# Kernel tuning notes

Hardware: AMD Instinct MI355X
Metric: run time of the kernel (lower is better)

The kernel has to match this reference:

```python
import jax, jax.numpy as jnp
import numpy as np
from math import sqrt

B, LQ, LKV = 4, 1024, 1024
QD = KD = VD = 1024
MODEL_DIM = 1024
H = 16
HD = MODEL_DIM // H  # per-head model_dim = 64


def setup_inputs() -> dict:
    key = jax.random.key(0)
    ks = jax.random.split(key, 10)
    s = 0.02
    return {
        "queries": jax.random.normal(ks[0], (B, LQ, QD), jnp.float32),
        "context": jax.random.normal(ks[1], (B, LKV, KD), jnp.float32),
        # stacked per-head linear weights (torch Linear: y = x @ W.T + b); store as [H, in, out]
        "Wq": jax.random.normal(ks[2], (H, QD, HD), jnp.float32) * s,
        "bq": jax.random.normal(ks[3], (H, HD), jnp.float32) * s,
        "Wk": jax.random.normal(ks[4], (KD, HD * 1 * H), jnp.float32).reshape(H, KD, HD) * s,
        "bk": jax.random.normal(ks[5], (H, HD), jnp.float32) * s,
        "Wv": jax.random.normal(ks[6], (H, VD, HD), jnp.float32) * s,
        "bv": jax.random.normal(ks[7], (H, HD), jnp.float32) * s,
        "Wo": jax.random.normal(ks[8], (H * HD, MODEL_DIM), jnp.float32) * s,
        "bo": jax.random.normal(ks[9], (MODEL_DIM,), jnp.float32) * s,
    }


def reference(queries, context, Wq, bq, Wk, bk, Wv, bv, Wo, bo):
    # queries: [B,Lq,Dq]; context: [B,Lkv,Dk]
    # Per-head projections, batched over heads (equivalent to the torch per-head loop).
    q = jnp.einsum("bld,hdm->bhlm", queries, Wq) + bq[None, :, None, :]  # [B,H,Lq,hd]
    k = jnp.einsum("bld,hdm->bhlm", context, Wk) + bk[None, :, None, :]  # [B,H,Lkv,hd]
    v = jnp.einsum("bld,hdm->bhlm", context, Wv) + bv[None, :, None, :]  # [B,H,Lkv,hd]

    scale = 1.0 / sqrt(HD)
    scores = jnp.einsum("bhqd,bhkd->bhqk", q, k) * scale  # [B,H,Lq,Lkv]
    att = jax.nn.softmax(scores, axis=-1)
    head_out = jnp.einsum("bhqk,bhkd->bhqd", att, v)  # [B,H,Lq,hd]

    # torch concatenates heads along the last dim in head order 0..H-1
    multi = head_out.transpose(0, 2, 1, 3).reshape(B, LQ, H * HD)
    residual = q.transpose(0, 2, 1, 3).reshape(B, LQ, H * HD)

    out = multi @ Wo + bo  # [B,Lq,model_dim]
    return out, residual
```

## Files before the change

kernel.cpp:

```cpp
#include <hip/hip_runtime.h>
#include <hip/hip_bf16.h>


typedef unsigned short u16;
typedef __attribute__((ext_vector_type(8))) short short8;
typedef __attribute__((ext_vector_type(4))) float f32x4;

__device__ __forceinline__ float bf2f(u16 u) {
    union { unsigned int i; float f; } c;
    c.i = ((unsigned int)u) << 16;
    return c.f;
}

__device__ __forceinline__ u16 f2bf(float f) {
    unsigned int x = __float_as_uint(f);
    unsigned int r = (x + 0x7fffu + ((x >> 16) & 1u)) >> 16;
    return (u16)r;
}

__device__ __forceinline__ void glds16(u16* lds, const u16* g) {
    __builtin_amdgcn_global_load_lds(
        (const __attribute__((address_space(1))) void*)g,
        (__attribute__((address_space(3))) void*)lds, 16, 0, 0);
}

__global__ __launch_bounds__(256) void cast_bf16_kernel(
    const float* __restrict__ q, const float* __restrict__ c,
    u16* __restrict__ oq, u16* __restrict__ oc)
{
    const float* in = blockIdx.y ? c : q;
    u16* out = blockIdx.y ? oc : oq;
    size_t i = ((size_t)blockIdx.x * 256 + threadIdx.x) * 8;
    float4 v0 = *(const float4*)(in + i);
    float4 v1 = *(const float4*)(in + i + 4);
    short8 p;
    p[0] = (short)f2bf(v0.x); p[1] = (short)f2bf(v0.y);
    p[2] = (short)f2bf(v0.z); p[3] = (short)f2bf(v0.w);
    p[4] = (short)f2bf(v1.x); p[5] = (short)f2bf(v1.y);
    p[6] = (short)f2bf(v1.z); p[7] = (short)f2bf(v1.w);
    *(short8*)(out + i) = p;
}

__global__ __launch_bounds__(256) void transpose_cast(
    const float* __restrict__ in, u16* __restrict__ out, int C, size_t matStride)
{
    __shared__ float ls[64][65];
    const int t = threadIdx.x;
    const size_t moff = (size_t)blockIdx.z * matStride;
    const int rt = blockIdx.x * 64, ct = blockIdx.y * 64;
    #pragma unroll
    for (int i = 0; i < 4; ++i) {
        int s = i * 256 + t;
        int row = s >> 4, chunk = s & 15;
        float4 v = *(const float4*)(in + moff + (size_t)(rt + row) * C + ct + chunk * 4);
        ls[row][chunk * 4 + 0] = v.x;
        ls[row][chunk * 4 + 1] = v.y;
        ls[row][chunk * 4 + 2] = v.z;
        ls[row][chunk * 4 + 3] = v.w;
    }
    __syncthreads();
    #pragma unroll
    for (int i = 0; i < 2; ++i) {
        int s = i * 256 + t;
        int n = s >> 3, kc = s & 7;
        short8 p;
        #pragma unroll
        for (int j = 0; j < 8; ++j) p[j] = (short)f2bf(ls[kc * 8 + j][n]);
        *(short8*)(out + moff + (size_t)(ct + n) * 1024 + rt + kc * 8) = p;
    }
}

__device__ __forceinline__ void gemm_core(
    const u16* __restrict__ A, const u16* __restrict__ Wt,
    int m0, u16* As, u16* Bs, f32x4 (&acc)[4][4])
{
    const int t = threadIdx.x;
    const int w = t >> 6, lane = t & 63;
    const int quad = lane >> 4, c = lane & 15;
    const int srow = w * 32 + (lane >> 2);
    const int sch = lane & 3;

    const u16* gA = A + (size_t)(m0 + srow) * 1024 + sch * 8;
    const u16* gB = Wt + (size_t)srow * 1024 + sch * 8;
    u16* lA = As + w * 32 * 32;
    u16* lB = Bs + w * 32 * 32;
    const u16* afr = As + ((w >> 1) * 64 + c) * 32 + quad * 8;
    const u16* bfr = Bs + ((w & 1) * 64 + c) * 32 + quad * 8;

    for (int kt = 0; kt < 1024; kt += 32) {
        glds16(lA,           gA + kt);
        glds16(lA + 16 * 32, gA + kt + 16 * 1024);
        glds16(lB,           gB + kt);
        glds16(lB + 16 * 32, gB + kt + 16 * 1024);
        __syncthreads();
        short8 af[4], bf[4];
        #pragma unroll
        for (int rs = 0; rs < 4; ++rs) af[rs] = *(const short8*)(afr + rs * 16 * 32);
        #pragma unroll
        for (int cs = 0; cs < 4; ++cs) bf[cs] = *(const short8*)(bfr + cs * 16 * 32);
        #pragma unroll
        for (int rs = 0; rs < 4; ++rs)
            #pragma unroll
            for (int cs = 0; cs < 4; ++cs)
                acc[rs][cs] = __builtin_amdgcn_mfma_f32_16x16x32_bf16(
                    af[rs], bf[cs], acc[rs][cs], 0, 0, 0);
        __syncthreads();
    }
}

__global__ __launch_bounds__(256, 3) void gemm_qkv(
    const u16* __restrict__ Aq, const u16* __restrict__ Ac,
    const u16* __restrict__ Wqt, const u16* __restrict__ Wkt,
    const u16* __restrict__ Wvt,
    const float* __restrict__ bq, const float* __restrict__ bk,
    const float* __restrict__ bv,
    u16* __restrict__ qws, u16* __restrict__ kws, u16* __restrict__ vtws,
    float* __restrict__ resid)
{
    __shared__ u16 As[128 * 32];
    __shared__ u16 Bs[128 * 32];
    const int n0 = blockIdx.x * 128, m0 = blockIdx.y * 128, z = blockIdx.z;
    const int t = threadIdx.x;
    const int w = t >> 6, lane = t & 63;
    const int quad = lane >> 4, c = lane & 15;

    const u16* A = (z == 0) ? Aq : Ac;
    const u16* Wt = ((z == 0) ? Wqt : (z == 1) ? Wkt : Wvt) + (size_t)n0 * 1024;
    const float* bias = (z == 0) ? bq : (z == 1) ? bk : bv;

    f32x4 acc[4][4] = {};
    gemm_core(A, Wt, m0, As, Bs, acc);

    const int h = blockIdx.x * 2 + (w & 1);
    float bb[4];
    #pragma unroll
    for (int cs = 0; cs < 4; ++cs) bb[cs] = bias[h * 64 + cs * 16 + c];

    if (z == 2) {
        #pragma unroll
        for (int rs = 0; rs < 4; ++rs) {
            const int l0 = m0 + (w >> 1) * 64 + rs * 16 + quad * 4;
            const int b = l0 >> 10, l = l0 & 1023;
            #pragma unroll
            for (int cs = 0; cs < 4; ++cs) {
                const int hd = cs * 16 + c;
                ushort4 pk;
                pk.x = f2bf(acc[rs][cs][0] + bb[cs]);
                pk.y = f2bf(acc[rs][cs][1] + bb[cs]);
                pk.z = f2bf(acc[rs][cs][2] + bb[cs]);
                pk.w = f2bf(acc[rs][cs][3] + bb[cs]);
                *(ushort4*)(vtws + ((size_t)(b * 16 + h) * 64 + hd) * 1024 + l) = pk;
            }
        }
    } else {
        u16* dst = (z == 0) ? qws : kws;
        const float scale = (z == 0) ? 0.125f : 1.0f;
        #pragma unroll
        for (int rs = 0; rs < 4; ++rs) {
            #pragma unroll
            for (int r = 0; r < 4; ++r) {
                const int row = m0 + (w >> 1) * 64 + rs * 16 + quad * 4 + r;
                const int b = row >> 10, l = row & 1023;
                u16* drow = dst + (((size_t)(b * 16 + h) * 1024) + l) * 64;
                float* rrow = (z == 0) ? (resid + (size_t)row * 1024 + h * 64) : nullptr;
                #pragma unroll
                for (int cs = 0; cs < 4; ++cs) {
                    float v = acc[rs][cs][r] + bb[cs];
                    drow[cs * 16 + c] = f2bf(v * scale);
                    if (z == 0) rrow[cs * 16 + c] = v;
                }
            }
        }
    }
}

__global__ __launch_bounds__(256, 3) void gemm_out(
    const u16* __restrict__ A, const u16* __restrict__ Wot,
    const float* __restrict__ bo, float* __restrict__ out)
{
    __shared__ u16 As[128 * 32];
    __shared__ u16 Bs[128 * 32];
    const int n0 = blockIdx.x * 128, m0 = blockIdx.y * 128;
    const int t = threadIdx.x;
    const int w = t >> 6, lane = t & 63;
    const int quad = lane >> 4, c = lane & 15;

    f32x4 acc[4][4] = {};
    gemm_core(A, Wot + (size_t)n0 * 1024, m0, As, Bs, acc);

    const int nb = n0 + (w & 1) * 64;
    float bb[4];
    #pragma unroll
    for (int cs = 0; cs < 4; ++cs) bb[cs] = bo[nb + cs * 16 + c];

    #pragma unroll
    for (int rs = 0; rs < 4; ++rs) {
        #pragma unroll
        for (int r = 0; r < 4; ++r) {
            const int row = m0 + (w >> 1) * 64 + rs * 16 + quad * 4 + r;
            float* orow = out + (size_t)row * 1024 + nb;
            #pragma unroll
            for (int cs = 0; cs < 4; ++cs)
                orow[cs * 16 + c] = acc[rs][cs][r] + bb[cs];
        }
    }
}

__global__ __launch_bounds__(256, 4) void attn_mfma(
    const u16* __restrict__ qws, const u16* __restrict__ kws,
    const u16* __restrict__ vtws, u16* __restrict__ multi)
{
    __shared__ u16 Ks[64 * 64];
    __shared__ u16 Vs[64 * 64];
    __shared__ u16 Ps[4][16 * 72];
    const int t = threadIdx.x;
    const int wave = t >> 6, lane = t & 63;
    const int quad = lane >> 4, c = lane & 15;
    const int bh = blockIdx.y, b = bh >> 4, h = bh & 15;
    const int q0 = blockIdx.x * 64 + wave * 16;

    const u16* qb = qws + ((size_t)bh * 1024 + q0) * 64;
    const u16* kb = kws + (size_t)bh * 65536;
    const u16* vb = vtws + (size_t)bh * 65536;

    short8 qa0 = *(const short8*)(qb + (size_t)c * 64 + quad * 8);
    short8 qa1 = *(const short8*)(qb + (size_t)c * 64 + 32 + quad * 8);

    const int srow = wave * 16 + (lane >> 3);
    const int gch = (lane & 7) ^ ((lane >> 3) & 7);
    u16* ldsK0 = Ks + (wave * 16) * 64;
    u16* ldsK1 = Ks + (wave * 16 + 8) * 64;
    u16* ldsV0 = Vs + (wave * 16) * 64;
    u16* ldsV1 = Vs + (wave * 16 + 8) * 64;
    const u16* gK0 = kb + (size_t)srow * 64 + gch * 8;
    const u16* gK1 = kb + (size_t)(srow + 8) * 64 + gch * 8;
    const u16* gV0 = vb + (size_t)srow * 1024 + gch * 8;
    const u16* gV1 = vb + (size_t)(srow + 8) * 1024 + gch * 8;

    f32x4 O[4] = {};
    float ps[4] = {0.f, 0.f, 0.f, 0.f};
    u16* pw = &Ps[wave][0];
    const int cx = c & 7;

    for (int kt = 0; kt < 1024; kt += 64) {
        glds16(ldsK0, gK0 + (size_t)kt * 64);
        glds16(ldsK1, gK1 + (size_t)kt * 64);
        glds16(ldsV0, gV0 + kt);
        glds16(ldsV1, gV1 + kt);
        __syncthreads();

        f32x4 s[4];
        #pragma unroll
        for (int nt = 0; nt < 4; ++nt) {
            const u16* kr = Ks + (nt * 16 + c) * 64;
            short8 kb0 = *(const short8*)(kr + ((quad ^ cx)) * 8);
            short8 kb1 = *(const short8*)(kr + (((4 + quad) ^ cx)) * 8);
            f32x4 z = {};
            z = __builtin_amdgcn_mfma_f32_16x16x32_bf16(qa0, kb0, z, 0, 0, 0);
            z = __builtin_amdgcn_mfma_f32_16x16x32_bf16(qa1, kb1, z, 0, 0, 0);
            s[nt] = z;
        }

        #pragma unroll
        for (int nt = 0; nt < 4; ++nt)
            #pragma unroll
            for (int r = 0; r < 4; ++r) {
                float p = __expf(s[nt][r]);
                ps[r] += p;
                pw[(quad * 4 + r) * 72 + nt * 16 + c] = (u16)(__float_as_uint(p) >> 16);
            }
        short8 pa0 = *(const short8*)(pw + c * 72 + quad * 8);
        short8 pa1 = *(const short8*)(pw + c * 72 + 32 + quad * 8);

        #pragma unroll
        for (int nt = 0; nt < 4; ++nt) {
            const u16* vr = Vs + (nt * 16 + c) * 64;
            short8 vb0 = *(const short8*)(vr + ((quad ^ cx)) * 8);
            short8 vb1 = *(const short8*)(vr + (((4 + quad) ^ cx)) * 8);
            O[nt] = __builtin_amdgcn_mfma_f32_16x16x32_bf16(pa0, vb0, O[nt], 0, 0, 0);
            O[nt] = __builtin_amdgcn_mfma_f32_16x16x32_bf16(pa1, vb1, O[nt], 0, 0, 0);
        }
        __syncthreads();
    }

    float inv[4];
    #pragma unroll
    for (int r = 0; r < 4; ++r) {
        float sum = ps[r];
        sum += __shfl_xor(sum, 1);
        sum += __shfl_xor(sum, 2);
        sum += __shfl_xor(sum, 4);
        sum += __shfl_xor(sum, 8);
        inv[r] = 1.0f / sum;
    }

    u16* ob = multi + ((size_t)b * 1024 + q0 + quad * 4) * 1024 + h * 64 + c;
    #pragma unroll
    for (int r = 0; r < 4; ++r) {
        u16* orow = ob + (size_t)r * 1024;
        orow[0]  = f2bf(O[0][r] * inv[r]);
        orow[16] = f2bf(O[1][r] * inv[r]);
        orow[32] = f2bf(O[2][r] * inv[r]);
        orow[48] = f2bf(O[3][r] * inv[r]);
    }
}

extern "C" void kernel_launch(void* const* d_in, const int* in_sizes, int n_in,
                              void* d_out, int out_size, void* d_ws, size_t ws_size,
                              hipStream_t stream) {
    const float* queries = (const float*)d_in[0];
    const float* context = (const float*)d_in[1];
    const float* Wq = (const float*)d_in[2];
    const float* bq = (const float*)d_in[3];
    const float* Wk = (const float*)d_in[4];
    const float* bk = (const float*)d_in[5];
    const float* Wv = (const float*)d_in[6];
    const float* bv = (const float*)d_in[7];
    const float* Wo = (const float*)d_in[8];
    const float* bo = (const float*)d_in[9];

    float* out = (float*)d_out;
    float* resid = out + (size_t)4 * 1024 * 1024;

    const size_t M1 = 1024 * 1024;
    u16* Aq   = (u16*)d_ws;
    u16* Ac   = Aq + 4 * M1;
    u16* Wqt  = Ac + 4 * M1;
    u16* Wkt  = Wqt + M1;
    u16* Wvt  = Wkt + M1;
    u16* Wot  = Wvt + M1;
    u16* qws  = Wot + M1;
    u16* kws  = qws + 4 * M1;
    u16* vtws = kws + 4 * M1;
    u16* mws  = vtws + 4 * M1;

    cast_bf16_kernel<<<dim3(2048, 2), 256, 0, stream>>>(queries, context, Aq, Ac);
    transpose_cast<<<dim3(16, 1, 16), 256, 0, stream>>>(Wq, Wqt, 64, 65536);
    transpose_cast<<<dim3(16, 1, 16), 256, 0, stream>>>(Wk, Wkt, 64, 65536);
    transpose_cast<<<dim3(16, 1, 16), 256, 0, stream>>>(Wv, Wvt, 64, 65536);
    transpose_cast<<<dim3(16, 16, 1), 256, 0, stream>>>(Wo, Wot, 1024, 0);
    gemm_qkv<<<dim3(8, 32, 3), 256, 0, stream>>>(Aq, Ac, Wqt, Wkt, Wvt,
                                                 bq, bk, bv, qws, kws, vtws, resid);
    attn_mfma<<<dim3(16, 64), 256, 0, stream>>>(qws, kws, vtws, mws);
    gemm_out<<<dim3(8, 32), 256, 0, stream>>>(mws, Wot, bo, out);
}
```

Baseline: 211.2 us.

## Fuse prep kernels, keep attention P in registers, retile output GEMM

Merges the input cast and four weight transpose-cast launches into one prep kernel, cutting launch overhead. The attention kernel computes S transposed (K as the A operand) and rearranges the exp'd probabilities into the PV operand with cross-lane shuffles, removing the LDS round trip for P. The row-sum reduction is simplified to match the new layout. The output GEMM moves to 128x64 tiles with an XCD-aware 1D block mapping to raise block count and L2 locality, at the cost of more A reloads and extra shuffle work in attention.

Result: no change. 212.0 us (+0.4%).

```diff
diff --git a/kernel.cpp b/kernel.cpp
--- a/kernel.cpp
+++ b/kernel.cpp
@@ -24,30 +24,44 @@
         (__attribute__((address_space(3))) void*)lds, 16, 0, 0);
 }
 
-__global__ __launch_bounds__(256) void cast_bf16_kernel(
-    const float* __restrict__ q, const float* __restrict__ c,
-    u16* __restrict__ oq, u16* __restrict__ oc)
-{
-    const float* in = blockIdx.y ? c : q;
-    u16* out = blockIdx.y ? oc : oq;
-    size_t i = ((size_t)blockIdx.x * 256 + threadIdx.x) * 8;
-    float4 v0 = *(const float4*)(in + i);
-    float4 v1 = *(const float4*)(in + i + 4);
-    short8 p;
-    p[0] = (short)f2bf(v0.x); p[1] = (short)f2bf(v0.y);
-    p[2] = (short)f2bf(v0.z); p[3] = (short)f2bf(v0.w);
-    p[4] = (short)f2bf(v1.x); p[5] = (short)f2bf(v1.y);
-    p[6] = (short)f2bf(v1.z); p[7] = (short)f2bf(v1.w);
-    *(short8*)(out + i) = p;
-}
-
-__global__ __launch_bounds__(256) void transpose_cast(
-    const float* __restrict__ in, u16* __restrict__ out, int C, size_t matStride)
+__global__ __launch_bounds__(256) void prep(
+    const float* __restrict__ q, const float* __restrict__ ctx,
+    const float* __restrict__ Wq, const float* __restrict__ Wk,
+    const float* __restrict__ Wv, const float* __restrict__ Wo,
+    u16* __restrict__ Aq, u16* __restrict__ Ac,
+    u16* __restrict__ Wqt, u16* __restrict__ Wkt,
+    u16* __restrict__ Wvt, u16* __restrict__ Wot)
 {
     __shared__ float ls[64][65];
     const int t = threadIdx.x;
-    const size_t moff = (size_t)blockIdx.z * matStride;
-    const int rt = blockIdx.x * 64, ct = blockIdx.y * 64;
+    int bid = blockIdx.x;
+
+    if (bid < 4096) {
+        const float* in = (bid < 2048) ? q : ctx;
+        u16* out = (bid < 2048) ? Aq : Ac;
+        size_t i = ((size_t)(bid & 2047) * 256 + t) * 8;
+        float4 v0 = *(const float4*)(in + i);
+        float4 v1 = *(const float4*)(in + i + 4);
+        short8 p;
+        p[0] = (short)f2bf(v0.x); p[1] = (short)f2bf(v0.y);
+        p[2] = (short)f2bf(v0.z); p[3] = (short)f2bf(v0.w);
+        p[4] = (short)f2bf(v1.x); p[5] = (short)f2bf(v1.y);
+        p[6] = (short)f2bf(v1.z); p[7] = (short)f2bf(v1.w);
+        *(short8*)(out + i) = p;
+        return;
+    }
+    bid -= 4096;
+    const float* in; u16* out; int C; size_t moff; int rt, ct;
+    if (bid < 768) {
+        const int m = bid >> 8, idx = bid & 255;
+        in = (m == 0) ? Wq : (m == 1) ? Wk : Wv;
+        out = (m == 0) ? Wqt : (m == 1) ? Wkt : Wvt;
+        C = 64; rt = (idx & 15) * 64; ct = 0; moff = (size_t)(idx >> 4) * 65536;
+    } else {
+        const int idx = bid - 768;
+        in = Wo; out = Wot; C = 1024; moff = 0;
+        rt = (idx & 15) * 64; ct = (idx >> 4) * 64;
+    }
     #pragma unroll
     for (int i = 0; i < 4; ++i) {
         int s = i * 256 + t;
@@ -179,19 +193,48 @@
     const float* __restrict__ bo, float* __restrict__ out)
 {
     __shared__ u16 As[128 * 32];
-    __shared__ u16 Bs[128 * 32];
-    const int n0 = blockIdx.x * 128, m0 = blockIdx.y * 128;
+    __shared__ u16 Bs[64 * 32];
+    const int f = blockIdx.x;
+    const int xcd = f & 7, k = f >> 3;
+    const int m0 = (xcd * 4 + (k & 3)) * 128;
+    const int n0 = (k >> 2) * 64;
     const int t = threadIdx.x;
     const int w = t >> 6, lane = t & 63;
     const int quad = lane >> 4, c = lane & 15;
 
-    f32x4 acc[4][4] = {};
-    gemm_core(A, Wot + (size_t)n0 * 1024, m0, As, Bs, acc);
-
-    const int nb = n0 + (w & 1) * 64;
-    float bb[4];
-    #pragma unroll
-    for (int cs = 0; cs < 4; ++cs) bb[cs] = bo[nb + cs * 16 + c];
+    const int arow = w * 32 + (lane >> 2), ach = lane & 3;
+    const int brow = w * 16 + (lane >> 2);
+    const u16* gA = A + (size_t)(m0 + arow) * 1024 + ach * 8;
+    const u16* gB = Wot + (size_t)(n0 + brow) * 1024 + ach * 8;
+    u16* lA = As + w * 32 * 32;
+    u16* lB = Bs + w * 16 * 32;
+    const u16* afr = As + ((w >> 1) * 64 + c) * 32 + quad * 8;
+    const u16* bfr = Bs + ((w & 1) * 32 + c) * 32 + quad * 8;
+
+    f32x4 acc[4][2] = {};
+    for (int kt = 0; kt < 1024; kt += 32) {
+        glds16(lA,           gA + kt);
+        glds16(lA + 16 * 32, gA + kt + 16 * 1024);
+        glds16(lB,           gB + kt);
+        __syncthreads();
+        short8 af[4], bf[2];
+        #pragma unroll
+        for (int rs = 0; rs < 4; ++rs) af[rs] = *(const short8*)(afr + rs * 16 * 32);
+        #pragma unroll
+        for (int cs = 0; cs < 2; ++cs) bf[cs] = *(const short8*)(bfr + cs * 16 * 32);
+        #pragma unroll
+        for (int rs = 0; rs < 4; ++rs)
+            #pragma unroll
+            for (int cs = 0; cs < 2; ++cs)
+                acc[rs][cs] = __builtin_amdgcn_mfma_f32_16x16x32_bf16(
+                    af[rs], bf[cs], acc[rs][cs], 0, 0, 0);
+        __syncthreads();
+    }
+
+    const int nb = n0 + (w & 1) * 32;
+    float bb[2];
+    #pragma unroll
+    for (int cs = 0; cs < 2; ++cs) bb[cs] = bo[nb + cs * 16 + c];
 
     #pragma unroll
     for (int rs = 0; rs < 4; ++rs) {
@@ -200,7 +243,7 @@
             const int row = m0 + (w >> 1) * 64 + rs * 16 + quad * 4 + r;
             float* orow = out + (size_t)row * 1024 + nb;
             #pragma unroll
-            for (int cs = 0; cs < 4; ++cs)
+            for (int cs = 0; cs < 2; ++cs)
                 orow[cs * 16 + c] = acc[rs][cs][r] + bb[cs];
         }
     }
@@ -212,7 +255,6 @@
 {
     __shared__ u16 Ks[64 * 64];
     __shared__ u16 Vs[64 * 64];
-    __shared__ u16 Ps[4][16 * 72];
     const int t = threadIdx.x;
     const int wave = t >> 6, lane = t & 63;
     const int quad = lane >> 4, c = lane & 15;
@@ -238,8 +280,7 @@
     const u16* gV1 = vb + (size_t)(srow + 8) * 1024 + gch * 8;
 
     f32x4 O[4] = {};
-    float ps[4] = {0.f, 0.f, 0.f, 0.f};
-    u16* pw = &Ps[wave][0];
+    float lsum = 0.f;
     const int cx = c & 7;
 
     for (int kt = 0; kt < 1024; kt += 64) {
@@ -249,50 +290,55 @@
         glds16(ldsV1, gV1 + kt);
         __syncthreads();
 
-        f32x4 s[4];
-        #pragma unroll
-        for (int nt = 0; nt < 4; ++nt) {
-            const u16* kr = Ks + (nt * 16 + c) * 64;
-            short8 kb0 = *(const short8*)(kr + ((quad ^ cx)) * 8);
-            short8 kb1 = *(const short8*)(kr + (((4 + quad) ^ cx)) * 8);
-            f32x4 z = {};
-            z = __builtin_amdgcn_mfma_f32_16x16x32_bf16(qa0, kb0, z, 0, 0, 0);
-            z = __builtin_amdgcn_mfma_f32_16x16x32_bf16(qa1, kb1, z, 0, 0, 0);
-            s[nt] = z;
+        #pragma unroll
+        for (int hb = 0; hb < 2; ++hb) {
+            const int kbase = hb * 32;
+            const u16* kr0 = Ks + (kbase + c) * 64;
+            const u16* kr1 = Ks + (kbase + 16 + c) * 64;
+            short8 kf00 = *(const short8*)(kr0 + (quad ^ cx) * 8);
+            short8 kf01 = *(const short8*)(kr0 + ((4 + quad) ^ cx) * 8);
+            short8 kf10 = *(const short8*)(kr1 + (quad ^ cx) * 8);
+            short8 kf11 = *(const short8*)(kr1 + ((4 + quad) ^ cx) * 8);
+
+            f32x4 st0 = {}, st1 = {};
+            st0 = __builtin_amdgcn_mfma_f32_16x16x32_bf16(kf00, qa0, st0, 0, 0, 0);
+            st0 = __builtin_amdgcn_mfma_f32_16x16x32_bf16(kf01, qa1, st0, 0, 0, 0);
+            st1 = __builtin_amdgcn_mfma_f32_16x16x32_bf16(kf10, qa0, st1, 0, 0, 0);
+            st1 = __builtin_amdgcn_mfma_f32_16x16x32_bf16(kf11, qa1, st1, 0, 0, 0);
+
+            f32x4 p0, p1;
+            #pragma unroll
+            for (int r = 0; r < 4; ++r) {
+                p0[r] = __expf(st0[r]);
+                p1[r] = __expf(st1[r]);
+                lsum += p0[r] + p1[r];
+            }
+
+            short8 pa;
+            #pragma unroll
+            for (int j = 0; j < 8; ++j) {
+                const int srcl = ((2 * quad + (j >> 2)) & 3) * 16 + c;
+                float v0 = __shfl(p0[j & 3], srcl);
+                float v1 = __shfl(p1[j & 3], srcl);
+                float v = (quad < 2) ? v0 : v1;
+                pa[j] = (short)(__float_as_uint(v) >> 16);
+            }
+
+            #pragma unroll
+            for (int nt = 0; nt < 4; ++nt) {
+                const u16* vr = Vs + (nt * 16 + c) * 64;
+                short8 vf = *(const short8*)(vr + ((hb * 4 + quad) ^ cx) * 8);
+                O[nt] = __builtin_amdgcn_mfma_f32_16x16x32_bf16(pa, vf, O[nt], 0, 0, 0);
+            }
         }
-
-        #pragma unroll
-        for (int nt = 0; nt < 4; ++nt)
-            #pragma unroll
-            for (int r = 0; r < 4; ++r) {
-                float p = __expf(s[nt][r]);
-                ps[r] += p;
-                pw[(quad * 4 + r) * 72 + nt * 16 + c] = (u16)(__float_as_uint(p) >> 16);
-            }
-        short8 pa0 = *(const short8*)(pw + c * 72 + quad * 8);
-        short8 pa1 = *(const short8*)(pw + c * 72 + 32 + quad * 8);
-
-        #pragma unroll
-        for (int nt = 0; nt < 4; ++nt) {
-            const u16* vr = Vs + (nt * 16 + c) * 64;
-            short8 vb0 = *(const short8*)(vr + ((quad ^ cx)) * 8);
-            short8 vb1 = *(const short8*)(vr + (((4 + quad) ^ cx)) * 8);
-            O[nt] = __builtin_amdgcn_mfma_f32_16x16x32_bf16(pa0, vb0, O[nt], 0, 0, 0);
-            O[nt] = __builtin_amdgcn_mfma_f32_16x16x32_bf16(pa1, vb1, O[nt], 0, 0, 0);
-        }
-        __syncthreads();
-    }
-
+        __syncthreads();
+    }
+
+    lsum += __shfl_xor(lsum, 16);
+    lsum += __shfl_xor(lsum, 32);
     float inv[4];
     #pragma unroll
-    for (int r = 0; r < 4; ++r) {
-        float sum = ps[r];
-        sum += __shfl_xor(sum, 1);
-        sum += __shfl_xor(sum, 2);
-        sum += __shfl_xor(sum, 4);
-        sum += __shfl_xor(sum, 8);
-        inv[r] = 1.0f / sum;
-    }
+    for (int r = 0; r < 4; ++r) inv[r] = 1.0f / __shfl(lsum, quad * 4 + r);
 
     u16* ob = multi + ((size_t)b * 1024 + q0 + quad * 4) * 1024 + h * 64 + c;
     #pragma unroll
@@ -334,13 +380,10 @@
     u16* vtws = kws + 4 * M1;
     u16* mws  = vtws + 4 * M1;
 
-    cast_bf16_kernel<<<dim3(2048, 2), 256, 0, stream>>>(queries, context, Aq, Ac);
-    transpose_cast<<<dim3(16, 1, 16), 256, 0, stream>>>(Wq, Wqt, 64, 65536);
-    transpose_cast<<<dim3(16, 1, 16), 256, 0, stream>>>(Wk, Wkt, 64, 65536);
-    transpose_cast<<<dim3(16, 1, 16), 256, 0, stream>>>(Wv, Wvt, 64, 65536);
-    transpose_cast<<<dim3(16, 16, 1), 256, 0, stream>>>(Wo, Wot, 1024, 0);
+    prep<<<5120, 256, 0, stream>>>(queries, context, Wq, Wk, Wv, Wo,
+                                   Aq, Ac, Wqt, Wkt, Wvt, Wot);
     gemm_qkv<<<dim3(8, 32, 3), 256, 0, stream>>>(Aq, Ac, Wqt, Wkt, Wvt,
                                                  bq, bk, bv, qws, kws, vtws, resid);
     attn_mfma<<<dim3(16, 64), 256, 0, stream>>>(qws, kws, vtws, mws);
-    gemm_out<<<dim3(8, 32), 256, 0, stream>>>(mws, Wot, bo, out);
-}
+    gemm_out<<<512, 256, 0, stream>>>(mws, Wot, bo, out);
+}
```
